# Kernel optimization log

Hardware: AMD Instinct MI355X
Metric: run time of the kernel (lower is better)

The kernel has to match this reference:

```python
import jax, jax.numpy as jnp
import numpy as np

B, N, M, K = 2, 4096, 512, 50
EMB, OUT = 512, 128
EPS = 1e-5


def _sqdist(a, b):
    # a: [B,P,D], b: [B,Q,D] -> squared euclidean distances [B,P,Q]
    return (jnp.sum(a * a, -1)[:, :, None] + jnp.sum(b * b, -1)[:, None, :]
            - 2.0 * jnp.einsum('bpd,bqd->bpq', a, b))


def _graph_feature(x, xg, k):
    # x: [B,D,N] points, xg: [B,D,M] grid -> edge features [B,2D,N,k]
    xt = x.transpose(0, 2, 1)   # [B,N,D]
    gt = xg.transpose(0, 2, 1)  # [B,M,D]
    nearest = jnp.argmin(_sqdist(xt, gt), axis=-1)               # [B,N] nearest grid pt per point
    _, nbr = jax.lax.top_k(-_sqdist(gt, gt), k)                  # [B,M,k] kNN within grid
    idx = jnp.take_along_axis(nbr, nearest[:, :, None], axis=1)  # [B,N,k]
    b = x.shape[0]
    feat = gt[jnp.arange(b)[:, None, None], idx]                 # [B,N,k,D] gathered grid feats
    feat = feat.at[:, :, 0, :].set(xt)                           # slot 0 <- point's own feature
    ctr = xt[:, :, None, :]
    out = jnp.concatenate([feat - ctr, jnp.broadcast_to(ctr, feat.shape)], axis=-1)
    return out.transpose(0, 3, 1, 2)                             # [B,2D,N,k]


def _lrelu(x):
    return jnp.where(x >= 0, x, 0.2 * x)


def _bn(y, g, bt, axes):
    # BatchNorm forward with batch statistics (torch training-mode math, biased var)
    m = jnp.mean(y, axis=axes, keepdims=True)
    v = jnp.mean((y - m) ** 2, axis=axes, keepdims=True)
    sh = [1] * y.ndim
    sh[1] = -1
    return (y - m) / jnp.sqrt(v + EPS) * g.reshape(sh) + bt.reshape(sh)


def _conv2(x, W, g, bt):
    # 1x1 Conv2d (no bias) + BN2d + LeakyReLU(0.2)
    return _lrelu(_bn(jnp.einsum('oc,bcnk->bonk', W, x), g, bt, (0, 2, 3)))


def _conv1(x, W, g, bt):
    # 1x1 Conv1d (no bias) + BN1d + LeakyReLU(0.2)
    return _lrelu(_bn(jnp.einsum('oc,bcn->bon', W, x), g, bt, (0, 2)))


def _forward(x, x_grid, FPS, W1, W2, W3, W4, W5, W6, W7, W8, W9,
             g1, g2, g3, g4, g5, g6, g7, g8,
             b1, b2, b3, b4, b5, b6, b7, b8):
    f = _graph_feature(x, x_grid, K)
    f = _conv2(f, W1, g1, b1)
    f = _conv2(f, W2, g2, b2)
    x1 = f.max(-1)                                               # [B,64,N]
    x1g = jnp.take_along_axis(x1, FPS[:, None, :], axis=2)       # [B,64,M]
    f = _graph_feature(x1, x1g, K)
    f = _conv2(f, W3, g3, b3)
    f = _conv2(f, W4, g4, b4)
    x2 = f.max(-1)
    x2g = jnp.take_along_axis(x2, FPS[:, None, :], axis=2)
    f = _graph_feature(x2, x2g, K)
    f = _conv2(f, W5, g5, b5)
    x3 = f.max(-1)
    x3g = jnp.take_along_axis(x3, FPS[:, None, :], axis=2)
    xg = jnp.concatenate([x1g, x2g, x3g], axis=1)                # [B,192,M]
    xg = _conv1(xg, W6, g6, b6)                                  # [B,EMB,M]
    xg = jnp.broadcast_to(xg.max(-1, keepdims=True), (x.shape[0], EMB, x.shape[2]))
    h = jnp.concatenate([xg, x1, x2, x3], axis=1)                # [B,EMB+192,N]
    h = _conv1(h, W7, g7, b7)
    h = _conv1(h, W8, g8, b8)
    h = jnp.einsum('oc,bcn->bon', W9, h)                         # final conv9, no BN/act
    return h.transpose(0, 2, 1)                                  # [B,N,OUT]


def setup_inputs() -> dict:
    key = jax.random.key(0)
    ks = jax.random.split(key, 32)
    def w(i, o, c):
        return jax.random.normal(ks[i], (o, c), jnp.float32) * 0.1
    inp = {
        'x': jax.random.normal(ks[0], (B, 3, N), jnp.float32),
        'x_grid': jax.random.normal(ks[1], (B, 3, M), jnp.float32),
        'FPS': jax.random.randint(ks[2], (B, M), 0, N),
        'W1': w(3, 64, 6), 'W2': w(4, 64, 64), 'W3': w(5, 64, 128),
        'W4': w(6, 64, 64), 'W5': w(7, 64, 128), 'W6': w(8, EMB, 192),
        'W7': w(9, 128, 192 + EMB), 'W8': w(10, 64, 128), 'W9': w(11, OUT, 64),
    }
    dims = [64, 64, 64, 64, 64, EMB, 128, 64]
    for j, d in enumerate(dims):
        inp[f'g{j+1}'] = 1.0 + 0.05 * jax.random.normal(ks[12 + j], (d,), jnp.float32)
        inp[f'b{j+1}'] = 0.05 * jax.random.normal(ks[20 + j], (d,), jnp.float32)
    return inp


def reference(x, x_grid, FPS, W1, W2, W3, W4, W5, W6, W7, W8, W9,
              g1, g2, g3, g4, g5, g6, g7, g8,
              b1, b2, b3, b4, b5, b6, b7, b8):
    return _forward(x, x_grid, FPS, W1, W2, W3, W4, W5, W6, W7, W8, W9,
                    g1, g2, g3, g4, g5, g6, g7, g8,
                    b1, b2, b3, b4, b5, b6, b7, b8)
```

## Files before the change

### kernel.cpp

```cpp
#include <hip/hip_runtime.h>
#include <hip/hip_bf16.h>

#define DEV __device__ __forceinline__
using bf16 = __hip_bfloat16;
using u16 = unsigned short;
using u64 = unsigned long long;

static constexpr int B_ = 2, N_ = 4096, M_ = 512, K_ = 50;
static constexpr int BN = B_ * N_;
static constexpr int BM = B_ * M_;
static constexpr float EPS_ = 1e-5f;

DEV float lrelu(float z) { return z < 0.f ? 0.2f * z : z; }
DEV int clampi(int v, int hi) { return ((unsigned)v < (unsigned)hi) ? v : 0; }

DEV u16 f2bfu(float f) {
    unsigned u = __float_as_uint(f);
    return (u16)((u + 0x7fffu + ((u >> 16) & 1u)) >> 16);
}
DEV float bfu2f(u16 h) { return __uint_as_float((unsigned)h << 16); }

typedef short bf8v __attribute__((ext_vector_type(8)));
typedef float f4v __attribute__((ext_vector_type(4)));

__global__ void k_detect(const unsigned short* __restrict__ xw, int* __restrict__ flag) {
    int t = threadIdx.x;
    int cnt = 0;
    for (int i = t; i < 4096; i += 256) {
        int e = (xw[i] >> 7) & 0xFF;
        if (e >= 100 && e <= 140) cnt++;
    }
    __shared__ int sh[256];
    sh[t] = cnt;
    __syncthreads();
    for (int s = 128; s; s >>= 1) { if (t < s) sh[t] += sh[t + s]; __syncthreads(); }
    if (t == 0) *flag = (sh[0] >= 3300) ? 1 : 0;
}

struct CvtDesc { const void* src; float* dst; int n; };
struct CvtArgs { CvtDesc d[25]; };
__global__ void k_convert(CvtArgs a, const int* __restrict__ flag) {
    CvtDesc dd = a.d[blockIdx.y];
    int i = blockIdx.x * 256 + threadIdx.x;
    if (i >= dd.n) return;
    float v = (*flag) ? __bfloat162float(((const bf16*)dd.src)[i])
                      : ((const float*)dd.src)[i];
    dd.dst[i] = v;
}

struct CvtT { const void* src; float* dst; int O; int C; int stride; int off; };
struct CvtTArgs { CvtT d[4]; };
__global__ void k_convT(CvtTArgs a, const int* __restrict__ flag) {
    CvtT dd = a.d[blockIdx.y];
    int idx = blockIdx.x * 256 + threadIdx.x;
    if (idx >= dd.O * dd.C) return;
    int c = idx / dd.O, o = idx % dd.O;
    int si = o * dd.stride + dd.off + c;
    float v = (*flag) ? __bfloat162float(((const bf16*)dd.src)[si])
                      : ((const float*)dd.src)[si];
    dd.dst[idx] = v;
}

__global__ void k_wfrag(const float* __restrict__ Wa, const float* __restrict__ Wb,
                        u16* __restrict__ fa, u16* __restrict__ fb) {
    const float* W = blockIdx.y ? Wb : Wa;
    u16* f = blockIdx.y ? fb : fa;
    int t = blockIdx.x * 256 + threadIdx.x;
    int j = t & 7, l = (t >> 3) & 63, s = (t >> 9) & 1, n = (t >> 10) & 3;
    int o = n * 16 + (l & 15);
    int c = s * 32 + (l >> 4) * 8 + j;
    float v = W[o * 64 + c];
    u16 hi = f2bfu(v);
    u16 lo = f2bfu(v - bfu2f(hi));
    f[t] = hi;
    f[4096 + t] = lo;
}

DEV float rdval(const void* p, int i, int isbf) {
    return isbf ? __bfloat162float(((const bf16*)p)[i]) : ((const float*)p)[i];
}
__global__ void k_transpose(const void* __restrict__ x, const void* __restrict__ xg,
                            const int* __restrict__ flag,
                            float* __restrict__ xt, float* __restrict__ gt,
                            float* __restrict__ gT3, float* __restrict__ gn) {
    int isbf = *flag;
    int idx = blockIdx.x * 256 + threadIdx.x;
    if (idx < BN * 3) {
        int c = idx / BN, i = idx % BN;
        int b = i / N_, n = i % N_;
        xt[i * 3 + c] = rdval(x, (b * 3 + c) * N_ + n, isbf);
    } else {
        int r = idx - BN * 3;
        if (r < BM) {
            int b = r / M_, m = r % M_;
            float s = 0.f;
            for (int c = 0; c < 3; c++) {
                float v = rdval(xg, (b * 3 + c) * M_ + m, isbf);
                gt[r * 3 + c] = v;
                gT3[(b * 3 + c) * M_ + m] = v;
                s = fmaf(v, v, s);
            }
            gn[r] = s;
        }
    }
}

DEV void nearest3_body(int blk, const float* __restrict__ q, const float* __restrict__ gt,
                       const float* __restrict__ gn, int* __restrict__ nearest) {
    int sub = threadIdx.x & 15;
    int pt = blk * 16 + (threadIdx.x >> 4);
    int b = pt >> 12;
    float q0 = q[pt * 3], q1 = q[pt * 3 + 1], q2 = q[pt * 3 + 2];
    float qn = q0 * q0 + q1 * q1 + q2 * q2;
    const float* gb = gt + (size_t)b * M_ * 3;
    const float* gnb = gn + b * M_;
    float best = 1e30f; int bi = 0x7fffffff;
    for (int j = 0; j < 32; j++) {
        int m = sub + 16 * j;
        float dot = q0 * gb[m * 3] + q1 * gb[m * 3 + 1] + q2 * gb[m * 3 + 2];
        float dv = qn + gnb[m] - 2.f * dot;
        if (dv < best || (dv == best && m < bi)) { best = dv; bi = m; }
    }
    for (int off = 8; off; off >>= 1) {
        float ov = __shfl_xor(best, off);
        int oi = __shfl_xor(bi, off);
        if (ov < best || (ov == best && oi < bi)) { best = ov; bi = oi; }
    }
    if (sub == 0) nearest[pt] = clampi(bi, M_);
}

DEV void nearest64_body_v4(int blk, const float* __restrict__ q,
                           const float* __restrict__ gT, const float* __restrict__ gn,
                           int* __restrict__ nearest,
                           float (*__restrict__ lg)[512], float (*__restrict__ ql)[64]) {
    int lane = threadIdx.x & 63;
    int tid = threadIdx.x;
    int w = __builtin_amdgcn_readfirstlane(threadIdx.x >> 6);
    int pt0 = blk * 16 + w * 4;
    int b = pt0 >> 12;
    const float* gTb = gT + (size_t)b * 64 * M_;
    {
        const float4* q4 = (const float4*)(q + (size_t)(blk * 16) * 64);
        ((float4*)ql)[tid] = q4[tid];
    }
    float qn[4] = {0.f, 0.f, 0.f, 0.f};
    float d[4][8] = {};
#pragma clang loop unroll(disable)
    for (int ch = 0; ch < 8; ch++) {
        __syncthreads();
        {
            const float4* src = (const float4*)(gTb + (size_t)ch * 8 * M_);
            float4* dst = (float4*)lg;
#pragma unroll
            for (int i = 0; i < 4; i++) {
                int idx = i * 256 + tid;
                dst[idx] = src[idx];
            }
        }
        __syncthreads();
#pragma unroll
        for (int j = 0; j < 8; j++) {
            float4 g0 = *(const float4*)&lg[j][4 * lane];
            float4 g1 = *(const float4*)&lg[j][256 + 4 * lane];
#pragma unroll
            for (int p = 0; p < 4; p++) {
                float qc = ql[w * 4 + p][ch * 8 + j];
                qn[p] = fmaf(qc, qc, qn[p]);
                d[p][0] = fmaf(qc, g0.x, d[p][0]); d[p][1] = fmaf(qc, g0.y, d[p][1]);
                d[p][2] = fmaf(qc, g0.z, d[p][2]); d[p][3] = fmaf(qc, g0.w, d[p][3]);
                d[p][4] = fmaf(qc, g1.x, d[p][4]); d[p][5] = fmaf(qc, g1.y, d[p][5]);
                d[p][6] = fmaf(qc, g1.z, d[p][6]); d[p][7] = fmaf(qc, g1.w, d[p][7]);
            }
        }
    }
    const float* gnb = gn + b * M_;
    float4 n0 = *(const float4*)(gnb + 4 * lane);
    float4 n1 = *(const float4*)(gnb + 256 + 4 * lane);
    float nn[8] = {n0.x, n0.y, n0.z, n0.w, n1.x, n1.y, n1.z, n1.w};
#pragma clang loop unroll(disable)
    for (int p = 0; p < 4; p++) {
        float best = 1e30f; int bi = 0;
#pragma unroll
        for (int i = 0; i < 8; i++) {
            int m = (i < 4) ? (4 * lane + i) : (256 + 4 * lane + i - 4);
            float dv = qn[p] + nn[i] - 2.f * d[p][i];
            if (dv < best || (dv == best && m < bi)) { best = dv; bi = m; }
        }
        for (int off = 32; off; off >>= 1) {
            float ov = __shfl_xor(best, off);
            int oi = __shfl_xor(bi, off);
            if (ov < best || (ov == best && oi < bi)) { best = ov; bi = oi; }
        }
        if (lane == 0) nearest[pt0 + p] = clampi(bi, M_);
    }
}

DEV void select50(const float dd[8], const int mreg[8], int lane,
                  int* __restrict__ rowp, int* __restrict__ idxrow) {
    u64 key[8];
#pragma unroll
    for (int i = 0; i < 8; i++) {
        unsigned u = __float_as_uint(dd[i]);
        if (u == 0x80000000u) u = 0u;
        u = (u & 0x80000000u) ? ~u : (u | 0x80000000u);
        key[i] = ((u64)u << 9) | (u64)(unsigned)mreg[i];
    }
    u64 kmin = key[0];
#pragma unroll
    for (int i = 1; i < 8; i++) kmin = key[i] < kmin ? key[i] : kmin;
    for (int off = 32; off; off >>= 1) {
        u64 o = __shfl_xor(kmin, off);
        kmin = o < kmin ? o : kmin;
    }
    u64 res = 0;
#pragma clang loop unroll(disable)
    for (int bit = 40; bit >= 0; --bit) {
        u64 t = res | ((u64)1 << bit);
        int c = 0;
#pragma unroll
        for (int i = 0; i < 8; i++) c += (key[i] < t) ? 1 : 0;
        u64 b0 = __ballot(c & 1), b1 = __ballot(c & 2), b2 = __ballot(c & 4), b3 = __ballot(c & 8);
        int tot = __popcll(b0) + 2 * __popcll(b1) + 4 * __popcll(b2) + 8 * __popcll(b3);
        if (tot <= K_ - 1) res = t;
    }
    int lc = 0, loc[8];
    bool sel[8];
#pragma unroll
    for (int i = 0; i < 8; i++) {
        sel[i] = (key[i] <= res) && (key[i] != kmin);
        loc[i] = lc;
        lc += sel[i] ? 1 : 0;
    }
    u64 lmask = ((u64)1 << lane) - 1;
    u64 c0 = __ballot(lc & 1), c1 = __ballot(lc & 2), c2 = __ballot(lc & 4), c3 = __ballot(lc & 8);
    int pre = __popcll(c0 & lmask) + 2 * __popcll(c1 & lmask)
            + 4 * __popcll(c2 & lmask) + 8 * __popcll(c3 & lmask);
#pragma unroll
    for (int i = 0; i < 8; i++) {
        if (key[i] == kmin) { rowp[0] = mreg[i]; idxrow[0] = mreg[i]; }
        if (sel[i]) { int p = 1 + pre + loc[i]; rowp[p] = mreg[i]; idxrow[p] = mreg[i]; }
    }
}

DEV void nbr3_body(int blk, const float* __restrict__ g, const float* __restrict__ gT,
                   const float* __restrict__ gn, const float* __restrict__ Pg,
                   int* __restrict__ nbr, float* __restrict__ T1, float* __restrict__ T2,
                   float* __restrict__ Mn, float* __restrict__ Mx,
                   int (*__restrict__ idxb)[64]) {
    int lane = threadIdx.x & 63, w = threadIdx.x >> 6;
    int row = blk * 4 + w;
    int b = row >> 9;
    const float* grow = g + (size_t)row * 3;
    float qn = gn[row];
    const float* gTb = gT + (size_t)b * 3 * M_;
    const float* gnb = gn + b * M_;
    float d[8] = {0.f, 0.f, 0.f, 0.f, 0.f, 0.f, 0.f, 0.f};
    {
        float qs[3];
#pragma unroll
        for (int c = 0; c < 3; c++) qs[c] = grow[c];
#pragma unroll
        for (int c = 0; c < 3; c++) {
            float qc = qs[c];
            float4 g0 = *(const float4*)(gTb + c * M_ + 4 * lane);
            float4 g1 = *(const float4*)(gTb + c * M_ + 256 + 4 * lane);
            d[0] = fmaf(qc, g0.x, d[0]); d[1] = fmaf(qc, g0.y, d[1]);
            d[2] = fmaf(qc, g0.z, d[2]); d[3] = fmaf(qc, g0.w, d[3]);
            d[4] = fmaf(qc, g1.x, d[4]); d[5] = fmaf(qc, g1.y, d[5]);
            d[6] = fmaf(qc, g1.z, d[6]); d[7] = fmaf(qc, g1.w, d[7]);
        }
    }
    float4 n0 = *(const float4*)(gnb + 4 * lane);
    float4 n1 = *(const float4*)(gnb + 256 + 4 * lane);
    float dd[8];
    dd[0] = qn + n0.x - 2.f * d[0]; dd[1] = qn + n0.y - 2.f * d[1];
    dd[2] = qn + n0.z - 2.f * d[2]; dd[3] = qn + n0.w - 2.f * d[3];
    dd[4] = qn + n1.x - 2.f * d[4]; dd[5] = qn + n1.y - 2.f * d[5];
    dd[6] = qn + n1.z - 2.f * d[6]; dd[7] = qn + n1.w - 2.f * d[7];
    int mreg[8];
#pragma unroll
    for (int i = 0; i < 8; i++) mreg[i] = (i < 4) ? (4 * lane + i) : (256 + 4 * lane + i - 4);
    select50(dd, mreg, lane, nbr + (size_t)row * K_, idxb[w]);
    int myIdx = idxb[w][lane];
    const float* Pgb = Pg + (size_t)b * M_ * 64;
    float t1 = 0.f, t2 = 0.f, mn = 1e30f, mx = -1e30f;
#pragma unroll 7
    for (int k = 1; k < K_; k++) {
        int idx = clampi(__shfl(myIdx, k), M_);
        float v = Pgb[(size_t)idx * 64 + lane];
        t1 += v; t2 = fmaf(v, v, t2);
        mn = fminf(mn, v); mx = fmaxf(mx, v);
    }
    size_t o = (size_t)row * 64 + lane;
    T1[o] = t1; T2[o] = t2; Mn[o] = mn; Mx[o] = mx;
}

DEV void nbr64_body(int blk, const float* __restrict__ g, const float* __restrict__ gT,
                    const float* __restrict__ gn, const float* __restrict__ Pg,
                    int* __restrict__ nbr, float* __restrict__ T1, float* __restrict__ T2,
                    float* __restrict__ Mn, float* __restrict__ Mx,
                    float (*__restrict__ lg)[512], float (*__restrict__ ql)[64],
                    int (*__restrict__ idxb)[64]) {
    int lane = threadIdx.x & 63, w = threadIdx.x >> 6;
    int tid = threadIdx.x;
    int row = blk * 4 + w;
    int b = row >> 9;
    float qn = gn[row];
    const float* gTb = gT + (size_t)b * 64 * M_;
    const float* gnb = gn + b * M_;
    if (tid < 64) {
        const float4* q4 = (const float4*)(g + (size_t)(blk * 4) * 64);
        ((float4*)ql)[tid] = q4[tid];
    }
    float d[8] = {0.f, 0.f, 0.f, 0.f, 0.f, 0.f, 0.f, 0.f};
#pragma clang loop unroll(disable)
    for (int ch = 0; ch < 8; ch++) {
        __syncthreads();
        {
            const float4* src = (const float4*)(gTb + (size_t)ch * 8 * M_);
            float4* dst = (float4*)lg;
#pragma unroll
            for (int i = 0; i < 4; i++) {
                int idx = i * 256 + tid;
                dst[idx] = src[idx];
            }
        }
        __syncthreads();
#pragma unroll
        for (int j = 0; j < 8; j++) {
            float qc = ql[w][ch * 8 + j];
            float4 g0 = *(const float4*)&lg[j][4 * lane];
            float4 g1 = *(const float4*)&lg[j][256 + 4 * lane];
            d[0] = fmaf(qc, g0.x, d[0]); d[1] = fmaf(qc, g0.y, d[1]);
            d[2] = fmaf(qc, g0.z, d[2]); d[3] = fmaf(qc, g0.w, d[3]);
            d[4] = fmaf(qc, g1.x, d[4]); d[5] = fmaf(qc, g1.y, d[5]);
            d[6] = fmaf(qc, g1.z, d[6]); d[7] = fmaf(qc, g1.w, d[7]);
        }
    }
    float4 n0 = *(const float4*)(gnb + 4 * lane);
    float4 n1 = *(const float4*)(gnb + 256 + 4 * lane);
    float dd[8];
    dd[0] = qn + n0.x - 2.f * d[0]; dd[1] = qn + n0.y - 2.f * d[1];
    dd[2] = qn + n0.z - 2.f * d[2]; dd[3] = qn + n0.w - 2.f * d[3];
    dd[4] = qn + n1.x - 2.f * d[4]; dd[5] = qn + n1.y - 2.f * d[5];
    dd[6] = qn + n1.z - 2.f * d[6]; dd[7] = qn + n1.w - 2.f * d[7];
    int mreg[8];
#pragma unroll
    for (int i = 0; i < 8; i++) mreg[i] = (i < 4) ? (4 * lane + i) : (256 + 4 * lane + i - 4);
    select50(dd, mreg, lane, nbr + (size_t)row * K_, idxb[w]);
    int myIdx = idxb[w][lane];
    const float* Pgb = Pg + (size_t)b * M_ * 64;
    float t1 = 0.f, t2 = 0.f, mn = 1e30f, mx = -1e30f;
#pragma unroll 7
    for (int k = 1; k < K_; k++) {
        int idx = clampi(__shfl(myIdx, k), M_);
        float v = Pgb[(size_t)idx * 64 + lane];
        t1 += v; t2 = fmaf(v, v, t2);
        mn = fminf(mn, v); mx = fmaxf(mx, v);
    }
    size_t o = (size_t)row * 64 + lane;
    T1[o] = t1; T2[o] = t2; Mn[o] = mn; Mx[o] = mx;
}

__global__ __launch_bounds__(256) void k_knn3(
    const float* __restrict__ q, const float* __restrict__ gt, const float* __restrict__ gT3,
    const float* __restrict__ gn, const float* __restrict__ Pg,
    int* __restrict__ nearest, int* __restrict__ nbr, float* __restrict__ T1,
    float* __restrict__ T2, float* __restrict__ Mn, float* __restrict__ Mx) {
    __shared__ int idxb[4][64];
    if (blockIdx.x < BN / 16) nearest3_body(blockIdx.x, q, gt, gn, nearest);
    else nbr3_body(blockIdx.x - BN / 16, gt, gT3, gn, Pg, nbr, T1, T2, Mn, Mx, idxb);
}
__global__ __launch_bounds__(256) void k_knn64(
    const float* __restrict__ q, const float* __restrict__ xgt, const float* __restrict__ gT,
    const float* __restrict__ gn, const float* __restrict__ Pg,
    int* __restrict__ nearest, int* __restrict__ nbr, float* __restrict__ T1,
    float* __restrict__ T2, float* __restrict__ Mn, float* __restrict__ Mx) {
    __shared__ float lg[8][512];
    __shared__ float ql[16][64];
    __shared__ int idxb[4][64];
    if (blockIdx.x < BN / 16) nearest64_body_v4(blockIdx.x, q, gT, gn, nearest, lg, ql);
    else nbr64_body(blockIdx.x - BN / 16, xgt, gT, gn, Pg, nbr, T1, T2, Mn, Mx, lg, ql, idxb);
}

#define STATS_STORE_64(s1v, s2v, partial)                                         \
    {                                                                             \
        __shared__ float r1_[256], r2_[256];                                      \
        r1_[threadIdx.x] = (s1v); r2_[threadIdx.x] = (s2v);                       \
        __syncthreads();                                                          \
        if (threadIdx.x < 64) {                                                   \
            int t_ = threadIdx.x;                                                 \
            float a1_ = r1_[t_] + r1_[t_ + 64] + r1_[t_ + 128] + r1_[t_ + 192];   \
            float a2_ = r2_[t_] + r2_[t_ + 64] + r2_[t_ + 128] + r2_[t_ + 192];   \
            float* sp_ = (partial) + (size_t)blockIdx.x * 128;                    \
            sp_[t_] = a1_; sp_[64 + t_] = a2_;                                    \
        }                                                                         \
    }

__global__ __launch_bounds__(256) void k_pgrid3(const float* __restrict__ g,
                                                const float* __restrict__ W1,
                                                float* __restrict__ Pg) {
    int lane = threadIdx.x & 63;
    int row = blockIdx.x * 4 + __builtin_amdgcn_readfirstlane(threadIdx.x >> 6);
    float c0 = g[row * 3], c1 = g[row * 3 + 1], c2 = g[row * 3 + 2];
    const float* wr = W1 + lane * 6;
    Pg[(size_t)row * 64 + lane] = fmaf(wr[0], c0, fmaf(wr[1], c1, wr[2] * c2));
}

__global__ __launch_bounds__(256) void k_gridprep(
    const float* __restrict__ xsrc, const int* __restrict__ FPS,
    const float* __restrict__ W1, float* __restrict__ xgt, float* __restrict__ gT,
    float* __restrict__ gn, float* __restrict__ Pg) {
    int lane = threadIdx.x & 63, w = threadIdx.x >> 6;
    int row = blockIdx.x * 4 + w;
    int b = row >> 9, m = row & 511;
    int src = b * N_ + clampi(FPS[row], N_);
    float ge = xsrc[(size_t)src * 64 + lane];
    xgt[(size_t)row * 64 + lane] = ge;
    gT[((size_t)b * 64 + lane) * M_ + m] = ge;
    const float* wr = W1 + lane * 128;
    float s = 0.f, acc = 0.f;
#pragma unroll
    for (int c = 0; c < 64; c++) {
        float vc = __shfl(ge, c);
        s = fmaf(vc, vc, s);
        acc = fmaf(wr[c], vc, acc);
    }
    Pg[(size_t)row * 64 + lane] = acc;
    if (lane == 0) gn[row] = s;
}

template <int D>
__global__ __launch_bounds__(256) void k_prep_stats(
    const float* __restrict__ q, const float* __restrict__ W1,
    const int* __restrict__ nearest, const float* __restrict__ T1,
    const float* __restrict__ T2, float* __restrict__ D0, float* __restrict__ S0,
    float* __restrict__ partial) {
    int lane = threadIdx.x & 63;
    int pt = blockIdx.x * 4 + __builtin_amdgcn_readfirstlane(threadIdx.x >> 6);
    int b = pt >> 12;
    float pa, pb;
    if constexpr (D == 3) {
        float c0 = q[pt * 3], c1 = q[pt * 3 + 1], c2 = q[pt * 3 + 2];
        const float* wr = W1 + lane * 6;
        pa = fmaf(wr[0], c0, fmaf(wr[1], c1, wr[2] * c2));
        pb = fmaf(wr[3], c0, fmaf(wr[4], c1, wr[5] * c2));
    } else {
        float ge = q[(size_t)pt * 64 + lane];
        const float* wr = W1 + lane * 128;
        pa = 0.f; pb = 0.f;
#pragma unroll
        for (int c = 0; c < 64; c++) {
            float sh = __shfl(ge, c);
            pa = fmaf(wr[c], sh, pa);
            pb = fmaf(wr[64 + c], sh, pb);
        }
    }
    float d0 = pb - pa, s0 = pb;
    size_t t = (size_t)pt * 64 + lane;
    D0[t] = d0;
    S0[t] = s0;
    size_t nr = ((size_t)b * M_ + clampi(nearest[pt], M_)) * 64 + lane;
    float t1 = T1[nr], t2 = T2[nr];
    float s1 = s0 + fmaf(49.f, d0, t1);
    float s2 = fmaf(s0, s0, fmaf(49.f * d0, d0, fmaf(2.f * d0, t1, t2)));
    STATS_STORE_64(s1, s2, partial)
}

__global__ void k_apply0(const float* __restrict__ D0, const float* __restrict__ S0,
                         const int* __restrict__ nearest, const float* __restrict__ Mn,
                         const float* __restrict__ Mx, const float* __restrict__ prm,
                         float* __restrict__ xout) {
    int t = blockIdx.x * 256 + threadIdx.x;
    int pt = t >> 6, o = t & 63;
    int b = pt >> 12;
    size_t nr = ((size_t)b * M_ + clampi(nearest[pt], M_)) * 64 + o;
    float d0 = D0[t], s0 = S0[t];
    float a = prm[o], sh = prm[64 + o];
    float v = a > 0.f ? fmaxf(s0, d0 + Mx[nr]) : fminf(s0, d0 + Mn[nr]);
    xout[t] = lrelu(fmaf(a, v, sh));
}

__global__ __launch_bounds__(256) void k_pass1_mfma(
    const float* __restrict__ Pg, const float* __restrict__ D0,
    const float* __restrict__ S0, const int* __restrict__ nearest,
    const int* __restrict__ nbr, const float* __restrict__ prm1,
    const u16* __restrict__ wf, float* __restrict__ partial,
    float* __restrict__ mn_out, float* __restrict__ mx_out) {
    __shared__ u16 Zs[2][2][4096];
    __shared__ float ls1[128], ls2[128];
    int l = threadIdx.x & 63;
    int w = threadIdx.x >> 6;
    int wp = w >> 1, nh = w & 1;
    bf8v whi[2][2], wlo[2][2];
#pragma unroll
    for (int nt = 0; nt < 2; nt++)
#pragma unroll
        for (int s = 0; s < 2; s++) {
            int fi = (((nh * 2 + nt) * 2 + s) * 64 + l) * 8;
            whi[nt][s] = *(const bf8v*)(wf + fi);
            wlo[nt][s] = *(const bf8v*)(wf + 4096 + fi);
        }
    {
        int tt = threadIdx.x & 127;
        int p = threadIdx.x >> 7;
        int k = tt & 63, ch = tt >> 6;
        int pt = blockIdx.x * 2 + p, b = pt >> 12;
        int nr = clampi(nearest[pt], M_);
        const int* nrow = nbr + ((size_t)b * M_ + nr) * K_;
        int idx = (k >= 1 && k < K_) ? clampi(nrow[k], M_) : 0;
        const float4* src = ((k == 0) ? (const float4*)(S0 + (size_t)pt * 64)
                                      : (const float4*)(Pg + ((size_t)b * M_ + idx) * 64)) + ch * 8;
        const float4* d4 = (const float4*)(D0 + (size_t)pt * 64) + ch * 8;
        const float4* a4 = (const float4*)(prm1) + ch * 8;
        const float4* s4 = (const float4*)(prm1 + 64) + ch * 8;
        float dscale = (k == 0) ? 0.f : 1.f;
        bool pad = (k >= K_);
        char* zh = (char*)&Zs[p][0][0];
        char* zl = (char*)&Zs[p][1][0];
        int swz = (k & 7) << 4;
#pragma unroll
        for (int q2 = 0; q2 < 4; q2++) {
            unsigned hv[4], lv[4];
#pragma unroll
            for (int h = 0; h < 2; h++) {
                float4 v = src[q2 * 2 + h], d = d4[q2 * 2 + h];
                float4 a = a4[q2 * 2 + h], s = s4[q2 * 2 + h];
                float z0 = lrelu(fmaf(a.x, fmaf(dscale, d.x, v.x), s.x));
                float z1 = lrelu(fmaf(a.y, fmaf(dscale, d.y, v.y), s.y));
                float z2 = lrelu(fmaf(a.z, fmaf(dscale, d.z, v.z), s.z));
                float z3 = lrelu(fmaf(a.w, fmaf(dscale, d.w, v.w), s.w));
                if (pad) { z0 = 0.f; z1 = 0.f; z2 = 0.f; z3 = 0.f; }
                unsigned h0 = f2bfu(z0), h1 = f2bfu(z1), h2 = f2bfu(z2), h3 = f2bfu(z3);
                unsigned l0 = f2bfu(z0 - bfu2f((u16)h0)), l1 = f2bfu(z1 - bfu2f((u16)h1));
                unsigned l2 = f2bfu(z2 - bfu2f((u16)h2)), l3 = f2bfu(z3 - bfu2f((u16)h3));
                hv[h * 2] = h0 | (h1 << 16); hv[h * 2 + 1] = h2 | (h3 << 16);
                lv[h * 2] = l0 | (l1 << 16); lv[h * 2 + 1] = l2 | (l3 << 16);
            }
            int ad = k * 128 + ((ch * 64 + q2 * 16) ^ swz);
            *(uint4*)(zh + ad) = make_uint4(hv[0], hv[1], hv[2], hv[3]);
            *(uint4*)(zl + ad) = make_uint4(lv[0], lv[1], lv[2], lv[3]);
        }
    }
    __syncthreads();
    int pt = blockIdx.x * 2 + wp;
    const char* zh = (const char*)&Zs[wp][0][0];
    const char* zl = (const char*)&Zs[wp][1][0];
    f4v acc[4][2] = {};
#pragma unroll
    for (int s = 0; s < 2; s++) {
        bf8v ah[4], al[4];
#pragma unroll
        for (int m = 0; m < 4; m++) {
            int row = m * 16 + (l & 15);
            int ad = row * 128 + (((s * 64) + ((l >> 4) * 16)) ^ ((row & 7) << 4));
            ah[m] = *(const bf8v*)(zh + ad);
            al[m] = *(const bf8v*)(zl + ad);
        }
#pragma unroll
        for (int m = 0; m < 4; m++)
#pragma unroll
            for (int nt = 0; nt < 2; nt++) {
                acc[m][nt] = __builtin_amdgcn_mfma_f32_16x16x32_bf16(ah[m], whi[nt][s], acc[m][nt], 0, 0, 0);
                acc[m][nt] = __builtin_amdgcn_mfma_f32_16x16x32_bf16(al[m], whi[nt][s], acc[m][nt], 0, 0, 0);
                acc[m][nt] = __builtin_amdgcn_mfma_f32_16x16x32_bf16(ah[m], wlo[nt][s], acc[m][nt], 0, 0, 0);
            }
    }
    int rg = (l >> 4) * 4;
#pragma unroll
    for (int nt = 0; nt < 2; nt++) {
        float s1 = 0.f, s2 = 0.f, mn = 1e30f, mx = -1e30f;
#pragma unroll
        for (int m = 0; m < 4; m++)
#pragma unroll
            for (int i = 0; i < 4; i++) {
                int kk = m * 16 + rg + i;
                float v = acc[m][nt][i];
                if (kk < K_) { s1 += v; s2 = fmaf(v, v, s2); mn = fminf(mn, v); mx = fmaxf(mx, v); }
            }
        for (int off = 16; off <= 32; off <<= 1) {
            s1 += __shfl_xor(s1, off); s2 += __shfl_xor(s2, off);
            mn = fminf(mn, __shfl_xor(mn, off)); mx = fmaxf(mx, __shfl_xor(mx, off));
        }
        if (l < 16) {
            int o = nh * 32 + nt * 16 + l;
            mn_out[(size_t)pt * 64 + o] = mn;
            mx_out[(size_t)pt * 64 + o] = mx;
            ls1[wp * 64 + o] = s1;
            ls2[wp * 64 + o] = s2;
        }
    }
    __syncthreads();
    if (threadIdx.x < 64) {
        int t = threadIdx.x;
        float* sp = partial + (size_t)blockIdx.x * 128;
        sp[t] = ls1[t] + ls1[64 + t];
        sp[64 + t] = ls2[t] + ls2[64 + t];
    }
}

__global__ void k_apply(const float* __restrict__ mn, const float* __restrict__ mx,
                        const float* __restrict__ prm, float* __restrict__ xout) {
    int t = blockIdx.x * 256 + threadIdx.x;
    int o = t & 63;
    float a = prm[o], sh = prm[64 + o];
    float v = a > 0.f ? mx[t] : mn[t];
    xout[t] = lrelu(fmaf(a, v, sh));
}

template <int NP, int O>
__global__ __launch_bounds__(256) void k_redfin(
    const float* __restrict__ partial, double* __restrict__ red,
    int* __restrict__ counter, int C,
    const float* __restrict__ g, const float* __restrict__ bt,
    float* __restrict__ prm) {
    constexpr int VALS = 2 * O;
    constexpr int G = NP / 32;
    int b = blockIdx.x;
    for (int v = threadIdx.x; v < VALS; v += 256) {
        const float* p = partial + (size_t)b * G * VALS + v;
        double s = 0.0;
#pragma unroll
        for (int k = 0; k < G; k++) s += p[(size_t)k * VALS];
        red[(size_t)b * VALS + v] = s;
    }
    __threadfence();
    __syncthreads();
    __shared__ bool isLast;
    if (threadIdx.x == 0) isLast = (atomicAdd(counter, 1) == 31);
    __syncthreads();
    if (!isLast) return;
    __threadfence();
    for (int o = threadIdx.x; o < O; o += 256) {
        double s1 = 0.0, s2 = 0.0;
#pragma unroll
        for (int k = 0; k < 32; k++) {
            s1 += red[(size_t)k * VALS + o];
            s2 += red[(size_t)k * VALS + O + o];
        }
        double m = s1 / C, var = s2 / C - m * m;
        if (var < 0) var = 0;
        float sc = g[o] / sqrtf((float)var + EPS_);
        prm[o] = sc;
        prm[O + o] = bt[o] - (float)m * sc;
    }
}

__global__ __launch_bounds__(256) void k_conv_w6(
    const float* __restrict__ x1gt, const float* __restrict__ x2gt,
    const float* __restrict__ x3t, const int* __restrict__ FPS,
    const float* __restrict__ W6t, float* __restrict__ y6, float* __restrict__ partial) {
    __shared__ float vl[4][192];
    int b = blockIdx.x / 128;
    int m0 = (blockIdx.x % 128) * 4;
    for (int i = threadIdx.x; i < 4 * 192; i += 256) {
        int mi = i / 192, c = i % 192;
        float v;
        if (c < 128) {
            const float* src = c < 64 ? x1gt : x2gt;
            v = src[((size_t)b * M_ + m0 + mi) * 64 + (c & 63)];
        } else {
            int s = b * N_ + clampi(FPS[b * M_ + m0 + mi], N_);
            v = x3t[(size_t)s * 64 + (c - 128)];
        }
        vl[mi][c] = v;
    }
    __syncthreads();
    float acc0[4] = {0}, acc1[4] = {0};
    int o0 = threadIdx.x, o1 = threadIdx.x + 256;
    for (int c = 0; c < 192; c++) {
        float w0 = W6t[c * 512 + o0];
        float w1 = W6t[c * 512 + o1];
#pragma unroll
        for (int m = 0; m < 4; m++) { float v = vl[m][c]; acc0[m] = fmaf(w0, v, acc0[m]); acc1[m] = fmaf(w1, v, acc1[m]); }
    }
    float s1a = 0, s2a = 0, s1b = 0, s2b = 0;
    for (int m = 0; m < 4; m++) {
        float ya = acc0[m], yb = acc1[m];
        y6[((size_t)b * M_ + m0 + m) * 512 + o0] = ya;
        y6[((size_t)b * M_ + m0 + m) * 512 + o1] = yb;
        s1a += ya; s2a = fmaf(ya, ya, s2a); s1b += yb; s2b = fmaf(yb, yb, s2b);
    }
    float* sp = partial + (size_t)blockIdx.x * 1024;
    sp[o0] = s1a; sp[512 + o0] = s2a;
    sp[o1] = s1b; sp[512 + o1] = s2b;
}

__global__ void k_maxM(const float* __restrict__ y6, const float* __restrict__ prm,
                       float* __restrict__ xgmax) {
    int blk = blockIdx.x;
    int b = blk >> 6;
    int obase = (blk & 63) << 3;
    int o = obase + (threadIdx.x & 7);
    int mg = threadIdx.x >> 3;
    float a = prm[o], sh = prm[512 + o];
    float mx = -1e30f;
    for (int m = mg; m < M_; m += 32)
        mx = fmaxf(mx, lrelu(fmaf(a, y6[((size_t)b * M_ + m) * 512 + o], sh)));
    __shared__ float red[256];
    red[threadIdx.x] = mx;
    __syncthreads();
    for (int s = 128; s >= 8; s >>= 1) {
        if (threadIdx.x < s) red[threadIdx.x] = fmaxf(red[threadIdx.x], red[threadIdx.x + s]);
        __syncthreads();
    }
    if (threadIdx.x < 8) xgmax[b * 512 + obase + threadIdx.x] = red[threadIdx.x];
}

__global__ __launch_bounds__(256) void k_p7(const float* __restrict__ xgmax,
                                            const float* __restrict__ W7,
                                            float* __restrict__ p7) {
    int lane = threadIdx.x & 63, w = threadIdx.x >> 6;
    int t = blockIdx.x * 4 + w;
    int b = t >> 7, o = t & 127;
    float acc = 0.f;
#pragma unroll
    for (int j = 0; j < 8; j++) {
        int c = j * 64 + lane;
        acc = fmaf(W7[o * 704 + c], xgmax[b * 512 + c], acc);
    }
    for (int off = 32; off; off >>= 1) acc += __shfl_xor(acc, off);
    if (lane == 0) p7[t] = acc;
}

__global__ __launch_bounds__(256) void k_conv_w7(
    const float* __restrict__ x1t, const float* __restrict__ x2t,
    const float* __restrict__ x3t, const float* __restrict__ p7,
    const float* __restrict__ W7vt, float* __restrict__ y7, float* __restrict__ partial) {
    __shared__ float vl[16][192];
    int item0 = blockIdx.x * 16;
    for (int i = threadIdx.x; i < 16 * 192; i += 256) {
        int it = i / 192, c = i % 192;
        const float* src = c < 64 ? x1t : (c < 128 ? x2t : x3t);
        vl[it][c] = src[((size_t)(item0 + it)) * 64 + (c & 63)];
    }
    __syncthreads();
    int o = threadIdx.x & 127, h = threadIdx.x >> 7;
    float acc[8] = {0};
    for (int c = 0; c < 192; c++) {
        float w = W7vt[c * 128 + o];
#pragma unroll
        for (int i = 0; i < 8; i++) acc[i] = fmaf(w, vl[h * 8 + i][c], acc[i]);
    }
    float s1 = 0, s2 = 0;
    for (int i = 0; i < 8; i++) {
        int item = item0 + h * 8 + i;
        int b = item / N_;
        float yv = p7[b * 128 + o] + acc[i];
        y7[(size_t)item * 128 + o] = yv;
        s1 += yv; s2 = fmaf(yv, yv, s2);
    }
    __shared__ float r1[256], r2[256];
    r1[threadIdx.x] = s1; r2[threadIdx.x] = s2;
    __syncthreads();
    if (threadIdx.x < 128) {
        float* sp = partial + (size_t)blockIdx.x * 256;
        sp[threadIdx.x] = r1[threadIdx.x] + r1[threadIdx.x + 128];
        sp[128 + threadIdx.x] = r2[threadIdx.x] + r2[threadIdx.x + 128];
    }
}

__global__ __launch_bounds__(256) void k_conv_w8(
    const float* __restrict__ y7, const float* __restrict__ prm7,
    const float* __restrict__ W8t, float* __restrict__ y8, float* __restrict__ partial) {
    int lane = threadIdx.x & 63;
    int item = blockIdx.x * 4 + (threadIdx.x >> 6);
    float W0[64], W1r[64];
#pragma unroll
    for (int c = 0; c < 64; c++) {
        W0[c] = W8t[c * 64 + lane];
        W1r[c] = W8t[(64 + c) * 64 + lane];
    }
    float a0 = prm7[lane], sh0 = prm7[128 + lane];
    float a1 = prm7[64 + lane], sh1 = prm7[128 + 64 + lane];
    float z0 = lrelu(fmaf(a0, y7[(size_t)item * 128 + lane], sh0));
    float z1 = lrelu(fmaf(a1, y7[(size_t)item * 128 + 64 + lane], sh1));
    float acc = 0.f;
#pragma unroll
    for (int c = 0; c < 64; c++) {
        acc = fmaf(W0[c], __shfl(z0, c), acc);
        acc = fmaf(W1r[c], __shfl(z1, c), acc);
    }
    y8[(size_t)item * 64 + lane] = acc;
    STATS_STORE_64(acc, acc * acc, partial)
}

__global__ __launch_bounds__(256) void k_final(
    const float* __restrict__ y8, const float* __restrict__ prm8,
    const float* __restrict__ W9t, void* __restrict__ out, const int* __restrict__ flag) {
    __shared__ float zl[2][64];
    int item0 = blockIdx.x * 2;
    if (threadIdx.x < 128) {
        int it = threadIdx.x >> 6, c = threadIdx.x & 63;
        float z = fmaf(prm8[c], y8[(size_t)(item0 + it) * 64 + c], prm8[64 + c]);
        zl[it][c] = lrelu(z);
    }
    __syncthreads();
    int it = threadIdx.x >> 7, o = threadIdx.x & 127;
    float acc = 0.f;
#pragma unroll
    for (int c = 0; c < 64; c++) acc = fmaf(W9t[c * 128 + o], zl[it][c], acc);
    size_t oi = (size_t)(item0 + it) * 128 + o;
    if (*flag) ((bf16*)out)[oi] = __float2bfloat16(acc);
    else ((float*)out)[oi] = acc;
}

extern "C" void kernel_launch(void* const* d_in, const int* in_sizes, int n_in,
                              void* d_out, int out_size, void* d_ws, size_t ws_size,
                              hipStream_t stream) {
    (void)in_sizes; (void)n_in; (void)out_size; (void)ws_size;
    const void* x = d_in[0];
    const void* xgrid = d_in[1];
    const int* FPS = (const int*)d_in[2];

    char* ws = (char*)d_ws;
    size_t off = 0;
    auto alloc = [&](size_t bytes) -> char* {
        char* p = ws + off;
        off = (off + bytes + 255) & ~(size_t)255;
        return p;
    };
    int* flag       = (int*)alloc(256);
    int* counters   = (int*)alloc(256);
    float* partials = (float*)alloc(4096 * 128 * sizeof(float));
    double* redbuf  = (double*)alloc(32 * 1024 * sizeof(double));
    float* prm      = (float*)alloc(8 * 1024 * sizeof(float));
    static const int wsz[9] = {384, 4096, 8192, 4096, 8192, 98304, 90112, 8192, 8192};
    static const int dims[8] = {64, 64, 64, 64, 64, 512, 128, 64};
    float* cW[9];
    for (int i = 0; i < 9; i++) cW[i] = (float*)alloc((size_t)wsz[i] * 4);
    float* cG[8];
    float* cB[8];
    for (int j = 0; j < 8; j++) {
        cG[j] = (float*)alloc((size_t)dims[j] * 4);
        cB[j] = (float*)alloc((size_t)dims[j] * 4);
    }
    float* W6t  = (float*)alloc((size_t)512 * 192 * 4);
    float* W7vt = (float*)alloc((size_t)128 * 192 * 4);
    float* W8t  = (float*)alloc((size_t)64 * 128 * 4);
    float* W9t  = (float*)alloc((size_t)128 * 64 * 4);
    u16* wf2    = (u16*)alloc((size_t)8192 * 2);
    u16* wf4    = (u16*)alloc((size_t)8192 * 2);
    float* xt    = (float*)alloc((size_t)BN * 3 * 4);
    float* gt    = (float*)alloc((size_t)BM * 3 * 4);
    float* gT3   = (float*)alloc((size_t)B_ * 3 * M_ * 4);
    float* gn    = (float*)alloc((size_t)BM * 4);
    int* nearest = (int*)alloc((size_t)BN * 4);
    int* nbr     = (int*)alloc((size_t)BM * K_ * 4);
    float* Pg    = (float*)alloc((size_t)BM * 64 * 4);
    float* x1t   = (float*)alloc((size_t)BN * 64 * 4);
    float* x2t   = (float*)alloc((size_t)BN * 64 * 4);
    float* x3t   = (float*)alloc((size_t)BN * 64 * 4);
    float* x1gt  = (float*)alloc((size_t)BM * 64 * 4);
    float* x2gt  = (float*)alloc((size_t)BM * 64 * 4);
    float* gT64  = (float*)alloc((size_t)B_ * 64 * M_ * 4);
    float* y6    = (float*)alloc((size_t)BM * 512 * 4);
    float* xgmax = (float*)alloc((size_t)B_ * 512 * 4);
    float* p7    = (float*)alloc((size_t)B_ * 128 * 4);
    float* y7    = (float*)alloc((size_t)BN * 128 * 4);
    float* y8    = (float*)alloc((size_t)BN * 64 * 4);
    float* D0b = y7;
    float* S0b = y7 + (size_t)BN * 64;
    float* mnb = y8;
    float* mxb = y6;
    float* T1b = y6;
    float* T2b = y6 + (size_t)BM * 64;
    float* Mnb = y6 + (size_t)2 * BM * 64;
    float* Mxb = y6 + (size_t)3 * BM * 64;

    hipMemsetAsync(counters, 0, 8 * sizeof(int), stream);
    k_detect<<<1, 256, 0, stream>>>((const unsigned short*)x, flag);

    CvtArgs ca;
    for (int i = 0; i < 9; i++) ca.d[i] = {d_in[3 + i], cW[i], wsz[i]};
    for (int j = 0; j < 8; j++) {
        ca.d[9 + 2 * j]     = {d_in[12 + 2 * j], cG[j], dims[j]};
        ca.d[9 + 2 * j + 1] = {d_in[13 + 2 * j], cB[j], dims[j]};
    }
    k_convert<<<dim3(384, 25), 256, 0, stream>>>(ca, flag);
    CvtTArgs ct;
    ct.d[0] = {d_in[8],  W6t,  512, 192, 192, 0};
    ct.d[1] = {d_in[9],  W7vt, 128, 192, 704, 512};
    ct.d[2] = {d_in[10], W8t,  64, 128, 128, 0};
    ct.d[3] = {d_in[11], W9t,  128, 64, 64, 0};
    k_convT<<<dim3(384, 4), 256, 0, stream>>>(ct, flag);
    k_wfrag<<<dim3(16, 2), 256, 0, stream>>>(cW[1], cW[3], wf2, wf4);
    k_transpose<<<(BN * 3 + BM + 255) / 256, 256, 0, stream>>>(x, xgrid, flag, xt, gt, gT3, gn);

    const int PG = BN / 4;
    const int EW = BN * 64 / 256;
    const int CK = BN * K_;
    const int KNNG = BN / 16 + BM / 4;

    k_pgrid3<<<BM / 4, 256, 0, stream>>>(gt, cW[0], Pg);
    k_knn3<<<KNNG, 256, 0, stream>>>(xt, gt, gT3, gn, Pg, nearest, nbr, T1b, T2b, Mnb, Mxb);
    k_prep_stats<3><<<PG, 256, 0, stream>>>(xt, cW[0], nearest, T1b, T2b, D0b, S0b, partials);
    k_redfin<2048, 64><<<32, 256, 0, stream>>>(partials, redbuf, counters + 0, CK, cG[0], cB[0], prm + 0 * 1024);
    k_pass1_mfma<<<BN / 2, 256, 0, stream>>>(Pg, D0b, S0b, nearest, nbr, prm + 0 * 1024, wf2, partials, mnb, mxb);
    k_redfin<4096, 64><<<32, 256, 0, stream>>>(partials, redbuf, counters + 1, CK, cG[1], cB[1], prm + 1 * 1024);
    k_apply<<<EW, 256, 0, stream>>>(mnb, mxb, prm + 1 * 1024, x1t);

    k_gridprep<<<BM / 4, 256, 0, stream>>>(x1t, FPS, cW[2], x1gt, gT64, gn, Pg);
    k_knn64<<<KNNG, 256, 0, stream>>>(x1t, x1gt, gT64, gn, Pg, nearest, nbr, T1b, T2b, Mnb, Mxb);
    k_prep_stats<64><<<PG, 256, 0, stream>>>(x1t, cW[2], nearest, T1b, T2b, D0b, S0b, partials);
    k_redfin<2048, 64><<<32, 256, 0, stream>>>(partials, redbuf, counters + 2, CK, cG[2], cB[2], prm + 2 * 1024);
    k_pass1_mfma<<<BN / 2, 256, 0, stream>>>(Pg, D0b, S0b, nearest, nbr, prm + 2 * 1024, wf4, partials, mnb, mxb);
    k_redfin<4096, 64><<<32, 256, 0, stream>>>(partials, redbuf, counters + 3, CK, cG[3], cB[3], prm + 3 * 1024);
    k_apply<<<EW, 256, 0, stream>>>(mnb, mxb, prm + 3 * 1024, x2t);

    k_gridprep<<<BM / 4, 256, 0, stream>>>(x2t, FPS, cW[4], x2gt, gT64, gn, Pg);
    k_knn64<<<KNNG, 256, 0, stream>>>(x2t, x2gt, gT64, gn, Pg, nearest, nbr, T1b, T2b, Mnb, Mxb);
    k_prep_stats<64><<<PG, 256, 0, stream>>>(x2t, cW[4], nearest, T1b, T2b, D0b, S0b, partials);
    k_redfin<2048, 64><<<32, 256, 0, stream>>>(partials, redbuf, counters + 4, CK, cG[4], cB[4], prm + 4 * 1024);
    k_apply0<<<EW, 256, 0, stream>>>(D0b, S0b, nearest, Mnb, Mxb, prm + 4 * 1024, x3t);

    k_conv_w6<<<BM / 4, 256, 0, stream>>>(x1gt, x2gt, x3t, FPS, W6t, y6, partials);
    k_redfin<256, 512><<<32, 256, 0, stream>>>(partials, redbuf, counters + 5, BM, cG[5], cB[5], prm + 5 * 1024);
    k_maxM<<<B_ * 64, 256, 0, stream>>>(y6, prm + 5 * 1024, xgmax);
    k_p7<<<64, 256, 0, stream>>>(xgmax, cW[6], p7);
    k_conv_w7<<<BN / 16, 256, 0, stream>>>(x1t, x2t, x3t, p7, W7vt, y7, partials);
    k_redfin<512, 128><<<32, 256, 0, stream>>>(partials, redbuf, counters + 6, BN, cG[6], cB[6], prm + 6 * 1024);
    k_conv_w8<<<BN / 4, 256, 0, stream>>>(y7, prm + 6 * 1024, W8t, y8, partials);
    k_redfin<2048, 64><<<32, 256, 0, stream>>>(partials, redbuf, counters + 7, BN, cG[7], cB[7], prm + 7 * 1024);
    k_final<<<BN / 2, 256, 0, stream>>>(y8, prm + 7 * 1024, W9t, d_out, flag);
}
```

Before: 467.0 us.

## Transpose W3/W5 for coalesced loads, precompute BN-affine grid buffer, reuse LDS

W3 and W5 are transposed once at setup so the per-lane weight reads in gridprep and prep_stats become coalesced across lanes instead of strided by 128. A new k_ubuf kernel folds the BN scale and shift into the grid projections ahead of time, which removes one FMA per element from the gathered path in pass1. The low bf16 residual now uses truncation instead of rounding, and the stats scratch arrays reuse the Zs shared buffer behind an added barrier. In exchange this adds an extra small kernel launch per layer, and truncating the low bf16 part slightly changes precision.

```diff
diff --git a/kernel.cpp b/kernel.cpp
--- a/kernel.cpp
+++ b/kernel.cpp
@@ -49,7 +49,7 @@
 }
 
 struct CvtT { const void* src; float* dst; int O; int C; int stride; int off; };
-struct CvtTArgs { CvtT d[4]; };
+struct CvtTArgs { CvtT d[6]; };
 __global__ void k_convT(CvtTArgs a, const int* __restrict__ flag) {
     CvtT dd = a.d[blockIdx.y];
     int idx = blockIdx.x * 256 + threadIdx.x;
@@ -74,6 +74,13 @@
     u16 lo = f2bfu(v - bfu2f(hi));
     f[t] = hi;
     f[4096 + t] = lo;
+}
+
+__global__ void k_ubuf(const float* __restrict__ Pg, const float* __restrict__ prm,
+                       float* __restrict__ ub) {
+    int t = blockIdx.x * 256 + threadIdx.x;
+    int c = t & 63;
+    ub[t] = fmaf(prm[c], Pg[t], prm[64 + c]);
 }
 
 DEV float rdval(const void* p, int i, int isbf) {
@@ -409,7 +416,7 @@
 
 __global__ __launch_bounds__(256) void k_gridprep(
     const float* __restrict__ xsrc, const int* __restrict__ FPS,
-    const float* __restrict__ W1, float* __restrict__ xgt, float* __restrict__ gT,
+    const float* __restrict__ Wt, float* __restrict__ xgt, float* __restrict__ gT,
     float* __restrict__ gn, float* __restrict__ Pg) {
     int lane = threadIdx.x & 63, w = threadIdx.x >> 6;
     int row = blockIdx.x * 4 + w;
@@ -418,13 +425,12 @@
     float ge = xsrc[(size_t)src * 64 + lane];
     xgt[(size_t)row * 64 + lane] = ge;
     gT[((size_t)b * 64 + lane) * M_ + m] = ge;
-    const float* wr = W1 + lane * 128;
     float s = 0.f, acc = 0.f;
 #pragma unroll
     for (int c = 0; c < 64; c++) {
         float vc = __shfl(ge, c);
         s = fmaf(vc, vc, s);
-        acc = fmaf(wr[c], vc, acc);
+        acc = fmaf(Wt[c * 64 + lane], vc, acc);
     }
     Pg[(size_t)row * 64 + lane] = acc;
     if (lane == 0) gn[row] = s;
@@ -447,13 +453,12 @@
         pb = fmaf(wr[3], c0, fmaf(wr[4], c1, wr[5] * c2));
     } else {
         float ge = q[(size_t)pt * 64 + lane];
-        const float* wr = W1 + lane * 128;
         pa = 0.f; pb = 0.f;
 #pragma unroll
         for (int c = 0; c < 64; c++) {
             float sh = __shfl(ge, c);
-            pa = fmaf(wr[c], sh, pa);
-            pb = fmaf(wr[64 + c], sh, pb);
+            pa = fmaf(W1[c * 64 + lane], sh, pa);
+            pb = fmaf(W1[(64 + c) * 64 + lane], sh, pb);
         }
     }
     float d0 = pb - pa, s0 = pb;
@@ -482,13 +487,15 @@
 }
 
 __global__ __launch_bounds__(256) void k_pass1_mfma(
-    const float* __restrict__ Pg, const float* __restrict__ D0,
+    const float* __restrict__ ub, const float* __restrict__ D0,
     const float* __restrict__ S0, const int* __restrict__ nearest,
     const int* __restrict__ nbr, const float* __restrict__ prm1,
-    const u16* __restrict__ wf, float* __restrict__ partial,
+    const u16* __restrict__ wf, const float* __restrict__ zero64,
+    float* __restrict__ partial,
     float* __restrict__ mn_out, float* __restrict__ mx_out) {
     __shared__ u16 Zs[2][2][4096];
-    __shared__ float ls1[128], ls2[128];
+    float* ls1 = (float*)&Zs[0][0][0];
+    float* ls2 = ls1 + 128;
     int l = threadIdx.x & 63;
     int w = threadIdx.x >> 6;
     int wp = w >> 1, nh = w & 1;
@@ -510,11 +517,11 @@
         const int* nrow = nbr + ((size_t)b * M_ + nr) * K_;
         int idx = (k >= 1 && k < K_) ? clampi(nrow[k], M_) : 0;
         const float4* src = ((k == 0) ? (const float4*)(S0 + (size_t)pt * 64)
-                                      : (const float4*)(Pg + ((size_t)b * M_ + idx) * 64)) + ch * 8;
-        const float4* d4 = (const float4*)(D0 + (size_t)pt * 64) + ch * 8;
+                                      : (const float4*)(ub + ((size_t)b * M_ + idx) * 64)) + ch * 8;
+        const float4* d4 = ((k == 0) ? (const float4*)zero64
+                                     : (const float4*)(D0 + (size_t)pt * 64)) + ch * 8;
         const float4* a4 = (const float4*)(prm1) + ch * 8;
         const float4* s4 = (const float4*)(prm1 + 64) + ch * 8;
-        float dscale = (k == 0) ? 0.f : 1.f;
         bool pad = (k >= K_);
         char* zh = (char*)&Zs[p][0][0];
         char* zl = (char*)&Zs[p][1][0];
@@ -524,16 +531,23 @@
             unsigned hv[4], lv[4];
 #pragma unroll
             for (int h = 0; h < 2; h++) {
-                float4 v = src[q2 * 2 + h], d = d4[q2 * 2 + h];
-                float4 a = a4[q2 * 2 + h], s = s4[q2 * 2 + h];
-                float z0 = lrelu(fmaf(a.x, fmaf(dscale, d.x, v.x), s.x));
-                float z1 = lrelu(fmaf(a.y, fmaf(dscale, d.y, v.y), s.y));
-                float z2 = lrelu(fmaf(a.z, fmaf(dscale, d.z, v.z), s.z));
-                float z3 = lrelu(fmaf(a.w, fmaf(dscale, d.w, v.w), s.w));
+                float4 u = src[q2 * 2 + h], d = d4[q2 * 2 + h];
+                float4 a = a4[q2 * 2 + h];
+                if (k == 0) {
+                    float4 s = s4[q2 * 2 + h];
+                    u.x = fmaf(a.x, u.x, s.x); u.y = fmaf(a.y, u.y, s.y);
+                    u.z = fmaf(a.z, u.z, s.z); u.w = fmaf(a.w, u.w, s.w);
+                }
+                float z0 = lrelu(fmaf(a.x, d.x, u.x));
+                float z1 = lrelu(fmaf(a.y, d.y, u.y));
+                float z2 = lrelu(fmaf(a.z, d.z, u.z));
+                float z3 = lrelu(fmaf(a.w, d.w, u.w));
                 if (pad) { z0 = 0.f; z1 = 0.f; z2 = 0.f; z3 = 0.f; }
                 unsigned h0 = f2bfu(z0), h1 = f2bfu(z1), h2 = f2bfu(z2), h3 = f2bfu(z3);
-                unsigned l0 = f2bfu(z0 - bfu2f((u16)h0)), l1 = f2bfu(z1 - bfu2f((u16)h1));
-                unsigned l2 = f2bfu(z2 - bfu2f((u16)h2)), l3 = f2bfu(z3 - bfu2f((u16)h3));
+                unsigned l0 = __float_as_uint(z0 - bfu2f((u16)h0)) >> 16;
+                unsigned l1 = __float_as_uint(z1 - bfu2f((u16)h1)) >> 16;
+                unsigned l2 = __float_as_uint(z2 - bfu2f((u16)h2)) >> 16;
+                unsigned l3 = __float_as_uint(z3 - bfu2f((u16)h3)) >> 16;
                 hv[h * 2] = h0 | (h1 << 16); hv[h * 2 + 1] = h2 | (h3 << 16);
                 lv[h * 2] = l0 | (l1 << 16); lv[h * 2 + 1] = l2 | (l3 << 16);
             }
@@ -566,6 +580,7 @@
                 acc[m][nt] = __builtin_amdgcn_mfma_f32_16x16x32_bf16(ah[m], wlo[nt][s], acc[m][nt], 0, 0, 0);
             }
     }
+    __syncthreads();
     int rg = (l >> 4) * 4;
 #pragma unroll
     for (int nt = 0; nt < 2; nt++) {
@@ -822,6 +837,7 @@
     };
     int* flag       = (int*)alloc(256);
     int* counters   = (int*)alloc(256);
+    float* zero64   = (float*)alloc(256);
     float* partials = (float*)alloc(4096 * 128 * sizeof(float));
     double* redbuf  = (double*)alloc(32 * 1024 * sizeof(double));
     float* prm      = (float*)alloc(8 * 1024 * sizeof(float));
@@ -839,6 +855,8 @@
     float* W7vt = (float*)alloc((size_t)128 * 192 * 4);
     float* W8t  = (float*)alloc((size_t)64 * 128 * 4);
     float* W9t  = (float*)alloc((size_t)128 * 64 * 4);
+    float* W3t  = (float*)alloc((size_t)64 * 128 * 4);
+    float* W5t  = (float*)alloc((size_t)64 * 128 * 4);
     u16* wf2    = (u16*)alloc((size_t)8192 * 2);
     u16* wf4    = (u16*)alloc((size_t)8192 * 2);
     float* xt    = (float*)alloc((size_t)BN * 3 * 4);
@@ -848,6 +866,7 @@
     int* nearest = (int*)alloc((size_t)BN * 4);
     int* nbr     = (int*)alloc((size_t)BM * K_ * 4);
     float* Pg    = (float*)alloc((size_t)BM * 64 * 4);
+    float* ubuf  = (float*)alloc((size_t)BM * 64 * 4);
     float* x1t   = (float*)alloc((size_t)BN * 64 * 4);
     float* x2t   = (float*)alloc((size_t)BN * 64 * 4);
     float* x3t   = (float*)alloc((size_t)BN * 64 * 4);
@@ -869,6 +888,7 @@
     float* Mxb = y6 + (size_t)3 * BM * 64;
 
     hipMemsetAsync(counters, 0, 8 * sizeof(int), stream);
+    hipMemsetAsync(zero64, 0, 256, stream);
     k_detect<<<1, 256, 0, stream>>>((const unsigned short*)x, flag);
 
     CvtArgs ca;
@@ -883,7 +903,9 @@
     ct.d[1] = {d_in[9],  W7vt, 128, 192, 704, 512};
     ct.d[2] = {d_in[10], W8t,  64, 128, 128, 0};
     ct.d[3] = {d_in[11], W9t,  128, 64, 64, 0};
-    k_convT<<<dim3(384, 4), 256, 0, stream>>>(ct, flag);
+    ct.d[4] = {d_in[5],  W3t,  64, 128, 128, 0};
+    ct.d[5] = {d_in[7],  W5t,  64, 128, 128, 0};
+    k_convT<<<dim3(384, 6), 256, 0, stream>>>(ct, flag);
     k_wfrag<<<dim3(16, 2), 256, 0, stream>>>(cW[1], cW[3], wf2, wf4);
     k_transpose<<<(BN * 3 + BM + 255) / 256, 256, 0, stream>>>(x, xgrid, flag, xt, gt, gT3, gn);
 
@@ -891,26 +913,29 @@
     const int EW = BN * 64 / 256;
     const int CK = BN * K_;
     const int KNNG = BN / 16 + BM / 4;
+    const int UBG = BM * 64 / 256;
 
     k_pgrid3<<<BM / 4, 256, 0, stream>>>(gt, cW[0], Pg);
     k_knn3<<<KNNG, 256, 0, stream>>>(xt, gt, gT3, gn, Pg, nearest, nbr, T1b, T2b, Mnb, Mxb);
     k_prep_stats<3><<<PG, 256, 0, stream>>>(xt, cW[0], nearest, T1b, T2b, D0b, S0b, partials);
     k_redfin<2048, 64><<<32, 256, 0, stream>>>(partials, redbuf, counters + 0, CK, cG[0], cB[0], prm + 0 * 1024);
-    k_pass1_mfma<<<BN / 2, 256, 0, stream>>>(Pg, D0b, S0b, nearest, nbr, prm + 0 * 1024, wf2, partials, mnb, mxb);
+    k_ubuf<<<UBG, 256, 0, stream>>>(Pg, prm + 0 * 1024, ubuf);
+    k_pass1_mfma<<<BN / 2, 256, 0, stream>>>(ubuf, D0b, S0b, nearest, nbr, prm + 0 * 1024, wf2, zero64, partials, mnb, mxb);
     k_redfin<4096, 64><<<32, 256, 0, stream>>>(partials, redbuf, counters + 1, CK, cG[1], cB[1], prm + 1 * 1024);
     k_apply<<<EW, 256, 0, stream>>>(mnb, mxb, prm + 1 * 1024, x1t);
 
-    k_gridprep<<<BM / 4, 256, 0, stream>>>(x1t, FPS, cW[2], x1gt, gT64, gn, Pg);
+    k_gridprep<<<BM / 4, 256, 0, stream>>>(x1t, FPS, W3t, x1gt, gT64, gn, Pg);
     k_knn64<<<KNNG, 256, 0, stream>>>(x1t, x1gt, gT64, gn, Pg, nearest, nbr, T1b, T2b, Mnb, Mxb);
-    k_prep_stats<64><<<PG, 256, 0, stream>>>(x1t, cW[2], nearest, T1b, T2b, D0b, S0b, partials);
+    k_prep_stats<64><<<PG, 256, 0, stream>>>(x1t, W3t, nearest, T1b, T2b, D0b, S0b, partials);
     k_redfin<2048, 64><<<32, 256, 0, stream>>>(partials, redbuf, counters + 2, CK, cG[2], cB[2], prm + 2 * 1024);
-    k_pass1_mfma<<<BN / 2, 256, 0, stream>>>(Pg, D0b, S0b, nearest, nbr, prm + 2 * 1024, wf4, partials, mnb, mxb);
+    k_ubuf<<<UBG, 256, 0, stream>>>(Pg, prm + 2 * 1024, ubuf);
+    k_pass1_mfma<<<BN / 2, 256, 0, stream>>>(ubuf, D0b, S0b, nearest, nbr, prm + 2 * 1024, wf4, zero64, partials, mnb, mxb);
     k_redfin<4096, 64><<<32, 256, 0, stream>>>(partials, redbuf, counters + 3, CK, cG[3], cB[3], prm + 3 * 1024);
     k_apply<<<EW, 256, 0, stream>>>(mnb, mxb, prm + 3 * 1024, x2t);
 
-    k_gridprep<<<BM / 4, 256, 0, stream>>>(x2t, FPS, cW[4], x2gt, gT64, gn, Pg);
+    k_gridprep<<<BM / 4, 256, 0, stream>>>(x2t, FPS, W5t, x2gt, gT64, gn, Pg);
     k_knn64<<<KNNG, 256, 0, stream>>>(x2t, x2gt, gT64, gn, Pg, nearest, nbr, T1b, T2b, Mnb, Mxb);
-    k_prep_stats<64><<<PG, 256, 0, stream>>>(x2t, cW[4], nearest, T1b, T2b, D0b, S0b, partials);
+    k_prep_stats<64><<<PG, 256, 0, stream>>>(x2t, W5t, nearest, T1b, T2b, D0b, S0b, partials);
     k_redfin<2048, 64><<<32, 256, 0, stream>>>(partials, redbuf, counters + 4, CK, cG[4], cB[4], prm + 4 * 1024);
     k_apply0<<<EW, 256, 0, stream>>>(D0b, S0b, nearest, Mnb, Mxb, prm + 4 * 1024, x3t);
 
```

Result: faster. 434.8 us (-6.9%).
